# Optimization experiments

Measured on AMD Instinct MI355X. Metric: run time of the kernel, lower is better.

The kernel has to match this reference:

```python
import jax, jax.numpy as jnp
from jax import lax
import numpy as np

N = 227328   # B(32) * T(64) * 111 ROIs, block-diagonal collated graph
E = 1000000  # thresholded sparse edges
H = 128      # hidden_dim
NB = 111     # brain ROIs per graph (hardcoded in source)
P = 40       # |perm| (pooled node subset)
MAXLEN = 10  # max_path_length
NSTART = 5   # top-5 start nodes


def setup_inputs() -> dict:
    key = jax.random.key(0)
    ks = jax.random.split(key, 12)
    s = 1.0 / np.sqrt(H)
    return dict(
        v=jax.random.normal(ks[0], (N, H), jnp.float32),
        edge_row=jax.random.randint(ks[1], (E,), 0, N, jnp.int32),
        edge_col=jax.random.randint(ks[2], (E,), 0, N, jnp.int32),
        W1=jax.random.normal(ks[3], (H, H), jnp.float32) * s,
        b1=jnp.zeros((H,), jnp.float32),
        g1=jnp.ones((H,), jnp.float32),
        be1=jnp.zeros((H,), jnp.float32),
        W2=jax.random.normal(ks[4], (H, H), jnp.float32) * s,
        b2=jnp.zeros((H,), jnp.float32),
        g2=jnp.ones((H,), jnp.float32),
        be2=jnp.zeros((H,), jnp.float32),
        epsilon=jnp.zeros((1, 1), jnp.float32),
        adj111=jax.random.randint(ks[5], (NB, NB), 0, 2, jnp.int32),
        node_scores=jax.random.normal(ks[6], (NB,), jnp.float32),
        node_feats=jax.random.normal(ks[7], (NB, H), jnp.float32),
        perm=jnp.arange(P, dtype=jnp.int32),
        x_small=jax.random.normal(ks[8], (P, H), jnp.float32),
    )


def _batchnorm(x, g, b, eps=1e-5):
    # BatchNorm1d in training mode: biased batch statistics over node dim
    m = x.mean(0)
    var = x.var(0)
    return g * (x - m) * lax.rsqrt(var + eps) + b


def _gin(v, row, col, epsilon, W1, b1, g1, be1, W2, b2, g2, be2):
    # torch.sparse.mm(a, v): agg[i] = sum_{j: a[i,j]=1} v[j]
    agg = jax.ops.segment_sum(v[col], row, num_segments=v.shape[0])
    h = agg + epsilon[0, 0] * v
    h = jax.nn.relu(_batchnorm(h @ W1 + b1, g1, be1))
    h = jax.nn.relu(_batchnorm(h @ W2 + b2, g2, be2))
    return h


def _biased_random_walk(adj, scores, x, feats, perm):
    soft = jax.nn.softmax(scores)
    order = jnp.argsort(-scores)              # nodes by descending score
    in_perm = jnp.isin(order, perm)
    pos = jnp.where(in_perm, jnp.arange(NB), NB)
    starts = order[jnp.argsort(pos)[:NSTART]]  # first 5 sorted nodes in perm
    start_ok = jnp.arange(NSTART) < jnp.minimum(jnp.sum(in_perm), NSTART)

    def walk_one(carry, se):
        all_visited, xc = carry
        start, ok = se
        skip = jnp.logical_or(~ok, all_visited[start])
        visited0 = all_visited.at[start].set(True)

        def step(c, _):
            cur, visited, alive = c
            nbr = (adj[cur] > 0) & (~visited)
            has = jnp.any(nbr) & alive
            nxt = jnp.argmax(jnp.where(nbr, soft, -jnp.inf))  # greedy by softmax score
            cur2 = jnp.where(has, nxt, cur)
            visited2 = jnp.where(has, visited.at[nxt].set(True), visited)
            return (cur2, visited2, has), (cur2, has)

        (_, visited_f, _), (pn, pv) = lax.scan(
            step, (start, visited0, True), None, length=MAXLEN - 1)
        path = jnp.concatenate([start[None], pn])           # [MAXLEN]
        valid = jnp.concatenate([jnp.array([True]), pv])
        w = jax.nn.softmax(jnp.where(valid, scores[path], -jnp.inf))
        fused = jnp.sum(w[:, None] * feats[path], axis=0)   # [H]
        idx = jnp.argmax(perm == start)
        do = (~skip) & jnp.any(perm == start)
        x_new = jnp.where(do, xc.at[idx].add(fused), xc)
        av_new = jnp.where(skip, all_visited, visited_f)
        return (av_new, x_new), None

    (_, x_out), _ = lax.scan(
        walk_one, (jnp.zeros((NB,), bool), x), (starts, start_ok))
    return x_out


def reference(v, edge_row, edge_col, W1, b1, g1, be1, W2, b2, g2, be2,
              epsilon, adj111, node_scores, node_feats, perm, x_small):
    gin_out = _gin(v, edge_row, edge_col, epsilon,
                   W1, b1, g1, be1, W2, b2, g2, be2)
    x_fused = _biased_random_walk(adj111, node_scores, x_small,
                                  node_feats, perm)
    return gin_out, x_fused
```

## Files before the change

### kernel.cpp

```cpp
#include <hip/hip_runtime.h>
#include <hip/hip_bf16.h>
#include <math.h>

#define N_NODES 227328
#define H_DIM 128
#define NB_ 111
#define P_ 40
#define MAXLEN_ 10
#define NSTART_ 5
#define NH (N_NODES * H_DIM)
#define SCAN_BLK 1024

typedef __attribute__((ext_vector_type(8))) short short8;
typedef __attribute__((ext_vector_type(4))) float f32x4;


__global__ __launch_bounds__(256) void k_zero(float* wsf, int* cnt, int n) {
    int gstride = gridDim.x * blockDim.x;
    for (int i = blockIdx.x * blockDim.x + threadIdx.x; i < n; i += gstride) cnt[i] = 0;
    if (blockIdx.x == 0)
        for (int i = threadIdx.x; i < 1280; i += 256) wsf[i] = 0.f;
}


__global__ __launch_bounds__(256) void k_hist(const int* __restrict__ erow, int* cnt, int E) {
    int stride = gridDim.x * blockDim.x;
    for (int e = blockIdx.x * blockDim.x + threadIdx.x; e < E; e += stride)
        atomicAdd(&cnt[erow[e]], 1);
}

__global__ __launch_bounds__(256) void k_scan1(const int* __restrict__ cnt, int* __restrict__ ptr,
                                               int* __restrict__ bsum, int n) {
    __shared__ int s_warp[4];
    int t = threadIdx.x;
    int base = blockIdx.x * SCAN_BLK + t * 4;
    int x0 = (base + 0 < n) ? cnt[base + 0] : 0;
    int x1 = (base + 1 < n) ? cnt[base + 1] : 0;
    int x2 = (base + 2 < n) ? cnt[base + 2] : 0;
    int x3 = (base + 3 < n) ? cnt[base + 3] : 0;
    int tsum = x0 + x1 + x2 + x3;
    int lane = t & 63, w = t >> 6;
    int v = tsum;
#pragma unroll
    for (int m = 1; m < 64; m <<= 1) {
        int o = __shfl_up(v, m, 64);
        if (lane >= m) v += o;
    }
    if (lane == 63) s_warp[w] = v;
    __syncthreads();
    int wadd = 0;
    for (int j = 0; j < w; j++) wadd += s_warp[j];
    int excl = v - tsum + wadd;
    if (base + 0 < n) ptr[base + 0] = excl;
    if (base + 1 < n) ptr[base + 1] = excl + x0;
    if (base + 2 < n) ptr[base + 2] = excl + x0 + x1;
    if (base + 3 < n) ptr[base + 3] = excl + x0 + x1 + x2;
    if (t == 0) bsum[blockIdx.x] = s_warp[0] + s_warp[1] + s_warp[2] + s_warp[3];
}

__global__ __launch_bounds__(256) void k_scan2(int* bsum, int nb) {
    __shared__ int s[256];
    int t = threadIdx.x;
    s[t] = (t < nb) ? bsum[t] : 0;
    __syncthreads();
    if (t == 0) {
        int acc = 0;
        for (int i = 0; i < nb; i++) { int x = s[i]; s[i] = acc; acc += x; }
    }
    __syncthreads();
    if (t < nb) bsum[t] = s[t];
}

__global__ __launch_bounds__(256) void k_scan3(int* __restrict__ ptr, const int* __restrict__ bsum,
                                               int* __restrict__ cur, int n, int E) {
    int stride = gridDim.x * blockDim.x;
    for (int i = blockIdx.x * blockDim.x + threadIdx.x; i < n; i += stride) {
        int p = ptr[i] + bsum[i / SCAN_BLK];
        ptr[i] = p;
        cur[i] = p;
    }
    if (blockIdx.x == 0 && threadIdx.x == 0) ptr[n] = E;
}

__global__ __launch_bounds__(256) void k_fill(const int* __restrict__ erow,
                                              const int* __restrict__ ecol,
                                              int* cur, int* __restrict__ col, int E) {
    int stride = gridDim.x * blockDim.x;
    for (int e = blockIdx.x * blockDim.x + threadIdx.x; e < E; e += stride) {
        int p = atomicAdd(&cur[erow[e]], 1);
        col[p] = ecol[e];
    }
}

__global__ __launch_bounds__(256) void k_agg(const float* __restrict__ v,
                                             const int* __restrict__ ptr,
                                             const int* __restrict__ col,
                                             const float* __restrict__ epsp,
                                             float* __restrict__ out, int n) {
    int r = (blockIdx.x * 256 + threadIdx.x) >> 6;
    int lane = threadIdx.x & 63;
    if (r >= n) return;
    float eps = epsp[0];
    float2 a = *((const float2*)(v + (size_t)r * H_DIM) + lane);
    float acx = eps * a.x, acy = eps * a.y;
    int s = ptr[r], e = ptr[r + 1];
    int i = s;
    for (; i + 4 <= e; i += 4) {
        int c0 = col[i], c1 = col[i + 1], c2 = col[i + 2], c3 = col[i + 3];
        float2 b0 = *((const float2*)(v + (size_t)c0 * H_DIM) + lane);
        float2 b1 = *((const float2*)(v + (size_t)c1 * H_DIM) + lane);
        float2 b2 = *((const float2*)(v + (size_t)c2 * H_DIM) + lane);
        float2 b3 = *((const float2*)(v + (size_t)c3 * H_DIM) + lane);
        acx += (b0.x + b1.x) + (b2.x + b3.x);
        acy += (b0.y + b1.y) + (b2.y + b3.y);
    }
    for (; i < e; i++) {
        int c = col[i];
        float2 b = *((const float2*)(v + (size_t)c * H_DIM) + lane);
        acx += b.x;
        acy += b.y;
    }
    *((float2*)(out + (size_t)r * H_DIM) + lane) = make_float2(acx, acy);
}


__global__ __launch_bounds__(256) void k_init(const float4* __restrict__ v4,
                                              const float* __restrict__ epsp,
                                              float4* __restrict__ out4, int n4) {
    float eps = epsp[0];
    int stride = gridDim.x * blockDim.x;
    for (int i = blockIdx.x * blockDim.x + threadIdx.x; i < n4; i += stride) {
        float4 a = v4[i];
        out4[i] = make_float4(eps * a.x, eps * a.y, eps * a.z, eps * a.w);
    }
}

__global__ __launch_bounds__(256) void k_scatter(const float* __restrict__ v,
                                                 const int* __restrict__ erow,
                                                 const int* __restrict__ ecol,
                                                 float* agg, int E) {
    int tid = blockIdx.x * blockDim.x + threadIdx.x;
    int lane = tid & 63;
    int wave = tid >> 6;
    int nwaves = (gridDim.x * blockDim.x) >> 6;
    for (int e = wave; e < E; e += nwaves) {
        int r = erow[e], c = ecol[e];
        const float2 val = *((const float2*)(v + (size_t)c * H_DIM) + lane);
        float* dst = agg + (size_t)r * H_DIM + lane * 2;
        unsafeAtomicAdd(dst, val.x);
        unsafeAtomicAdd(dst + 1, val.y);
    }
}


__device__ inline void split8(const float* xs, short8& hi, short8& lo) {
#pragma unroll
    for (int e = 0; e < 8; e++) {
        unsigned u = __float_as_uint(xs[e]);
        hi[e] = (short)(unsigned short)(u >> 16);
        float hf = __uint_as_float(u & 0xFFFF0000u);
        lo[e] = (short)(unsigned short)(__float_as_uint(xs[e] - hf) >> 16);
    }
}

template <int BN>
__global__ __launch_bounds__(256, 2) void k_gemm_mfma(
        const float* __restrict__ A, float* __restrict__ C,
        const float* __restrict__ W, const float* __restrict__ bias,
        const float* __restrict__ scl_in, const float* __restrict__ of_in,
        float* __restrict__ sums, float* __restrict__ sumsq) {
    __shared__ unsigned short Whi[128 * 136];
    __shared__ unsigned short Wlo[128 * 136];
    __shared__ float scof[256];
    __shared__ float stats[2][4][128];

    const int t = threadIdx.x;
    const int w = t >> 6;
    const int l = t & 63;
    const int n = l & 15;
    const int g = l >> 4;
    const size_t row0 = (size_t)blockIdx.x * 128 + w * 32;

#pragma unroll 8
    for (int it = 0; it < 64; ++it) {
        int k = it * 2 + (t >> 7);
        int nn = t & 127;
        float wv = W[k * 128 + nn];
        unsigned u = __float_as_uint(wv);
        Whi[nn * 136 + k] = (unsigned short)(u >> 16);
        float hf = __uint_as_float(u & 0xFFFF0000u);
        Wlo[nn * 136 + k] = (unsigned short)(__float_as_uint(wv - hf) >> 16);
    }
    if (BN && t < 128) { scof[t] = scl_in[t]; scof[128 + t] = of_in[t]; }
    __syncthreads();

    float breg[8];
#pragma unroll
    for (int cb = 0; cb < 8; cb++) breg[cb] = bias[cb * 16 + n];

    f32x4 acc[2][8];
#pragma unroll
    for (int rf = 0; rf < 2; rf++)
#pragma unroll
        for (int cb = 0; cb < 8; cb++) acc[rf][cb] = (f32x4){0.f, 0.f, 0.f, 0.f};

    const float* Arow0 = A + (row0 + n) * H_DIM;
    const float* Arow1 = A + (row0 + 16 + n) * H_DIM;

#pragma unroll
    for (int kb = 0; kb < 4; kb++) {
        const int k0 = kb * 32 + g * 8;
        float4 x00 = *(const float4*)(Arow0 + k0);
        float4 x01 = *(const float4*)(Arow0 + k0 + 4);
        float4 x10 = *(const float4*)(Arow1 + k0);
        float4 x11 = *(const float4*)(Arow1 + k0 + 4);
        float xs0[8] = {x00.x, x00.y, x00.z, x00.w, x01.x, x01.y, x01.z, x01.w};
        float xs1[8] = {x10.x, x10.y, x10.z, x10.w, x11.x, x11.y, x11.z, x11.w};
        if (BN) {
            float sc[8], of[8];
            float4 sa = *(const float4*)(scof + k0);
            float4 sb = *(const float4*)(scof + k0 + 4);
            float4 oa = *(const float4*)(scof + 128 + k0);
            float4 ob = *(const float4*)(scof + 128 + k0 + 4);
            sc[0] = sa.x; sc[1] = sa.y; sc[2] = sa.z; sc[3] = sa.w;
            sc[4] = sb.x; sc[5] = sb.y; sc[6] = sb.z; sc[7] = sb.w;
            of[0] = oa.x; of[1] = oa.y; of[2] = oa.z; of[3] = oa.w;
            of[4] = ob.x; of[5] = ob.y; of[6] = ob.z; of[7] = ob.w;
#pragma unroll
            for (int e = 0; e < 8; e++) {
                xs0[e] = fmaxf(fmaf(xs0[e], sc[e], of[e]), 0.f);
                xs1[e] = fmaxf(fmaf(xs1[e], sc[e], of[e]), 0.f);
            }
        }
        short8 ah0, al0, ah1, al1;
        split8(xs0, ah0, al0);
        split8(xs1, ah1, al1);

        short8 wh[8], wl[8];
        const int wb = n * 136 + kb * 32 + g * 8;
#pragma unroll
        for (int cb = 0; cb < 8; cb++) {
            wh[cb] = *(const short8*)(Whi + cb * 2176 + wb);
            wl[cb] = *(const short8*)(Wlo + cb * 2176 + wb);
        }
#pragma unroll
        for (int cb = 0; cb < 8; cb++) {
            acc[0][cb] = __builtin_amdgcn_mfma_f32_16x16x32_bf16(ah0, wh[cb], acc[0][cb], 0, 0, 0);
            acc[1][cb] = __builtin_amdgcn_mfma_f32_16x16x32_bf16(ah1, wh[cb], acc[1][cb], 0, 0, 0);
            acc[0][cb] = __builtin_amdgcn_mfma_f32_16x16x32_bf16(al0, wh[cb], acc[0][cb], 0, 0, 0);
            acc[1][cb] = __builtin_amdgcn_mfma_f32_16x16x32_bf16(al1, wh[cb], acc[1][cb], 0, 0, 0);
            acc[0][cb] = __builtin_amdgcn_mfma_f32_16x16x32_bf16(ah0, wl[cb], acc[0][cb], 0, 0, 0);
            acc[1][cb] = __builtin_amdgcn_mfma_f32_16x16x32_bf16(ah1, wl[cb], acc[1][cb], 0, 0, 0);
        }
    }

    float s[8], s2[8];
#pragma unroll
    for (int cb = 0; cb < 8; cb++) { s[cb] = 0.f; s2[cb] = 0.f; }
#pragma unroll
    for (int cb = 0; cb < 8; cb++) {
        const int c = cb * 16 + n;
#pragma unroll
        for (int rf = 0; rf < 2; rf++) {
            f32x4 o = acc[rf][cb];
            const size_t rbase = (row0 + rf * 16 + g * 4) * H_DIM + c;
#pragma unroll
            for (int r = 0; r < 4; r++) {
                float val = o[r] + breg[cb];
                C[rbase + (size_t)r * H_DIM] = val;
                s[cb] += val;
                s2[cb] += val * val;
            }
        }
    }
#pragma unroll
    for (int cb = 0; cb < 8; cb++) {
        s[cb] += __shfl_xor(s[cb], 16, 64);
        s[cb] += __shfl_xor(s[cb], 32, 64);
        s2[cb] += __shfl_xor(s2[cb], 16, 64);
        s2[cb] += __shfl_xor(s2[cb], 32, 64);
    }
    if (g == 0) {
#pragma unroll
        for (int cb = 0; cb < 8; cb++) {
            stats[0][w][cb * 16 + n] = s[cb];
            stats[1][w][cb * 16 + n] = s2[cb];
        }
    }
    __syncthreads();
    if (t < 128) {
        float S  = stats[0][0][t] + stats[0][1][t] + stats[0][2][t] + stats[0][3][t];
        float S2 = stats[1][0][t] + stats[1][1][t] + stats[1][2][t] + stats[1][3][t];
        unsafeAtomicAdd(sums + t, S);
        unsafeAtomicAdd(sumsq + t, S2);
    }
}

__global__ void k_finalize(const float* __restrict__ sums, const float* __restrict__ sumsq,
                           float* __restrict__ mean, float* __restrict__ scl,
                           float* __restrict__ of,
                           const float* __restrict__ g, const float* __restrict__ beta,
                           float invN) {
    int t = threadIdx.x;
    if (t < H_DIM) {
        float m = sums[t] * invN;
        float var = sumsq[t] * invN - m * m;
        float sc = g[t] * rsqrtf(var + 1e-5f);
        mean[t] = m;
        scl[t] = sc;
        of[t] = beta[t] - m * sc;
    }
}


__device__ inline float block_max4(float v, int t, float* s_r) {
#pragma unroll
    for (int m = 1; m < 64; m <<= 1) v = fmaxf(v, __shfl_xor(v, m, 64));
    if ((t & 63) == 0) s_r[t >> 6] = v;
    __syncthreads();
    float r = fmaxf(fmaxf(s_r[0], s_r[1]), fmaxf(s_r[2], s_r[3]));
    __syncthreads();
    return r;
}

__device__ inline float block_sum4(float v, int t, float* s_r) {
#pragma unroll
    for (int m = 1; m < 64; m <<= 1) v += __shfl_xor(v, m, 64);
    if ((t & 63) == 0) s_r[t >> 6] = v;
    __syncthreads();
    float r = (s_r[0] + s_r[1]) + (s_r[2] + s_r[3]);
    __syncthreads();
    return r;
}

__device__ inline void block_argmax4(float v, int idx, int t, float* s_rv, int* s_ri,
                                     float* outv, int* outi) {
#pragma unroll
    for (int m = 1; m < 64; m <<= 1) {
        float ov = __shfl_xor(v, m, 64);
        int oi = __shfl_xor(idx, m, 64);
        if (ov > v || (ov == v && oi < idx)) { v = ov; idx = oi; }
    }
    if ((t & 63) == 0) { s_rv[t >> 6] = v; s_ri[t >> 6] = idx; }
    __syncthreads();
    float bv = s_rv[0];
    int bi = s_ri[0];
#pragma unroll
    for (int j = 1; j < 4; j++) {
        float ov = s_rv[j];
        int oi = s_ri[j];
        if (ov > bv || (ov == bv && oi < bi)) { bv = ov; bi = oi; }
    }
    *outv = bv;
    *outi = bi;
    __syncthreads();
}

__global__ __launch_bounds__(256) void k_bnwalk(
        float4* y4, const float* __restrict__ scl, const float* __restrict__ of, int n4,
        const int* __restrict__ adj, const float* __restrict__ scores,
        const float* __restrict__ feats, const int* __restrict__ perm,
        const float* __restrict__ xs, float* __restrict__ outw) {
    __shared__ int s_adj[NB_ * NB_];
    __shared__ float s_scores[NB_], s_soft[NB_];
    __shared__ int s_perm[P_];
    __shared__ unsigned char s_inperm[NB_], s_sel[NB_], s_allvis[NB_], s_vis[NB_];
    __shared__ int s_starts[NSTART_];
    __shared__ int s_path[MAXLEN_];
    __shared__ unsigned char s_valid[MAXLEN_];
    __shared__ float s_w[MAXLEN_];
    __shared__ int s_cur, s_alive, s_do, s_idx, s_skip;
    __shared__ float s_rv[4];
    __shared__ int s_ri[4];

    const int t = threadIdx.x;

    if (blockIdx.x != 0) {
        int stride = (gridDim.x - 1) * 256;
        for (int i = (blockIdx.x - 1) * 256 + t; i < n4; i += stride) {
            int c = (i & 31) * 4;
            float4 a = y4[i];
            a.x = fmaxf(fmaf(a.x, scl[c + 0], of[c + 0]), 0.f);
            a.y = fmaxf(fmaf(a.y, scl[c + 1], of[c + 1]), 0.f);
            a.z = fmaxf(fmaf(a.z, scl[c + 2], of[c + 2]), 0.f);
            a.w = fmaxf(fmaf(a.w, scl[c + 3], of[c + 3]), 0.f);
            y4[i] = a;
        }
        return;
    }

    for (int i = t; i < P_ * H_DIM; i += 256) outw[i] = xs[i];
    for (int i = t; i < NB_ * NB_; i += 256) s_adj[i] = adj[i];
    if (t < P_) s_perm[t] = perm[t];
    if (t < NB_) { s_scores[t] = scores[t]; s_allvis[t] = 0; s_sel[t] = 0; }
    __syncthreads();
    if (t < NB_) {
        unsigned char inp = 0;
        for (int j = 0; j < P_; j++) inp |= (s_perm[j] == t) ? 1 : 0;
        s_inperm[t] = inp;
    }
    __syncthreads();

    float myv = (t < NB_) ? s_scores[t] : -INFINITY;
    float mx = block_max4(myv, t, s_rv);
    float e = (t < NB_) ? expf(s_scores[t] - mx) : 0.f;
    float ssum = block_sum4(e, t, s_rv);
    if (t < NB_) s_soft[t] = e / ssum;

    float ninf = block_sum4((t < NB_ && s_inperm[t]) ? 1.f : 0.f, t, s_rv);
    int nin = (int)(ninf + 0.5f);
    int nok = nin < NSTART_ ? nin : NSTART_;
    __syncthreads();

    for (int r = 0; r < NSTART_; r++) {
        bool useIn = (r < nin);
        bool elig = (t < NB_) && !s_sel[t] && (((s_inperm[t] != 0)) == useIn);
        float v = elig ? s_scores[t] : -INFINITY;
        float mv; int mi;
        block_argmax4(v, elig ? t : 0x7fffffff, t, s_rv, s_ri, &mv, &mi);
        if (t == 0) s_starts[r] = mi;
        if (t == mi && t < NB_) s_sel[t] = 1;
        __syncthreads();
    }

    for (int s = 0; s < NSTART_; s++) {
        if (t == 0) {
            int start = s_starts[s];
            int ok = (s < nok) ? 1 : 0;
            int skip = (!ok) || s_allvis[start];
            s_skip = skip;
            s_cur = start;
            s_alive = 1;
            s_path[0] = start;
            s_valid[0] = 1;
            int idx = 0, found = 0;
            for (int j = 0; j < P_; j++)
                if (!found && s_perm[j] == start) { idx = j; found = 1; }
            s_idx = idx;
            s_do = (!skip) && found;
        }
        __syncthreads();
        if (t < NB_) s_vis[t] = s_allvis[t];
        __syncthreads();
        if (t == 0) s_vis[s_cur] = 1;
        __syncthreads();

        for (int st = 1; st < MAXLEN_; st++) {
            int cur = s_cur;
            int alive = s_alive;
            bool elig = (t < NB_) && alive && (s_adj[cur * NB_ + t] > 0) && (!s_vis[t]);
            float v = elig ? s_soft[t] : -INFINITY;
            float mv; int mi;
            block_argmax4(v, elig ? t : 0x7fffffff, t, s_rv, s_ri, &mv, &mi);
            if (t == 0) {
                int has = (mv > -INFINITY) ? 1 : 0;
                if (has) { s_cur = mi; s_vis[mi] = 1; }
                s_path[st] = has ? mi : cur;
                s_valid[st] = (unsigned char)has;
                s_alive = has;
            }
            __syncthreads();
        }

        if (t == 0) {
            float mxw = -INFINITY;
            for (int st = 0; st < MAXLEN_; st++)
                if (s_valid[st]) mxw = fmaxf(mxw, s_scores[s_path[st]]);
            float sw = 0.f;
            for (int st = 0; st < MAXLEN_; st++) {
                float ev = s_valid[st] ? expf(s_scores[s_path[st]] - mxw) : 0.f;
                s_w[st] = ev; sw += ev;
            }
            float inv = 1.f / sw;
            for (int st = 0; st < MAXLEN_; st++) s_w[st] *= inv;
        }
        __syncthreads();
        if (s_do && t < H_DIM) {
            float acc = 0.f;
            for (int st = 0; st < MAXLEN_; st++)
                acc += s_w[st] * feats[s_path[st] * H_DIM + t];
            outw[s_idx * H_DIM + t] += acc;
        }
        __syncthreads();
        if (!s_skip && t < NB_) s_allvis[t] = s_vis[t];
        __syncthreads();
    }
}


extern "C" void kernel_launch(void* const* d_in, const int* in_sizes, int n_in,
                              void* d_out, int out_size, void* d_ws, size_t ws_size,
                              hipStream_t stream) {
    const float* v    = (const float*)d_in[0];
    const int*   erow = (const int*)d_in[1];
    const int*   ecol = (const int*)d_in[2];
    const float* W1   = (const float*)d_in[3];
    const float* b1   = (const float*)d_in[4];
    const float* g1   = (const float*)d_in[5];
    const float* be1  = (const float*)d_in[6];
    const float* W2   = (const float*)d_in[7];
    const float* b2   = (const float*)d_in[8];
    const float* g2   = (const float*)d_in[9];
    const float* be2  = (const float*)d_in[10];
    const float* epsp = (const float*)d_in[11];
    const int*   adj  = (const int*)d_in[12];
    const float* scr  = (const float*)d_in[13];
    const float* fts  = (const float*)d_in[14];
    const int*   perm = (const int*)d_in[15];
    const float* xs   = (const float*)d_in[16];

    float* out = (float*)d_out;
    float* wsf = (float*)d_ws;
    float* sums1 = wsf,        *sumsq1 = wsf + 128,  *mean1 = wsf + 256,  *scl1 = wsf + 384,  *of1 = wsf + 512;
    float* sums2 = wsf + 640,  *sumsq2 = wsf + 768,  *mean2 = wsf + 896,  *scl2 = wsf + 1024, *of2 = wsf + 1152;

    const int E  = in_sizes[1];
    const int N  = N_NODES;
    const int n4 = NH / 4;

    int* ws_i = (int*)(wsf + 1280);
    int* cnt  = ws_i;
    int* ptr  = ws_i + (N + 1);
    int* cur  = ws_i + 2 * (N + 1);
    int* col  = ws_i + 3 * (N + 1);
    size_t need = 1280 * 4 + (size_t)(3 * (N + 1) + E) * 4;

    if (ws_size >= need) {
        const int nb = (N + SCAN_BLK - 1) / SCAN_BLK;
        k_zero<<<512, 256, 0, stream>>>(wsf, cnt, N + 1);
        k_hist<<<1024, 256, 0, stream>>>(erow, cnt, E);
        k_scan1<<<nb, 256, 0, stream>>>(cnt, ptr, cur , N);
        k_scan2<<<1, 256, 0, stream>>>(cur, nb);
        k_scan3<<<512, 256, 0, stream>>>(ptr, cur, cnt , N, E);
        k_fill<<<1024, 256, 0, stream>>>(erow, ecol, cnt, col, E);
        k_agg<<<N / 4, 256, 0, stream>>>(v, ptr, col, epsp, out, N);
    } else {
        k_zero<<<512, 256, 0, stream>>>(wsf, cnt, 0);
        k_init<<<2048, 256, 0, stream>>>((const float4*)v, epsp, (float4*)out, n4);
        k_scatter<<<4096, 256, 0, stream>>>(v, erow, ecol, out, E);
    }

    k_gemm_mfma<0><<<N / 128, 256, 0, stream>>>(out, out, W1, b1, nullptr, nullptr,
                                                sums1, sumsq1);
    k_finalize<<<1, 128, 0, stream>>>(sums1, sumsq1, mean1, scl1, of1, g1, be1, 1.f / N);
    k_gemm_mfma<1><<<N / 128, 256, 0, stream>>>(out, out, W2, b2, scl1, of1,
                                                sums2, sumsq2);
    k_finalize<<<1, 128, 0, stream>>>(sums2, sumsq2, mean2, scl2, of2, g2, be2, 1.f / N);
    k_bnwalk<<<2049, 256, 0, stream>>>((float4*)out, scl2, of2, n4,
                                       adj, scr, fts, perm, xs, out + NH);
}
```

Baseline: 655.5 us.

## Gather neighbor features from a bf16 copy and prefetch GEMM A tiles

Adds a kernel that converts v to a bf16 copy in workspace, and switches the CSR aggregation to gather neighbor rows from that copy with an 8-wide unroll, halving gather bytes per edge. The GEMM kernel now loads W with vectorized float4 reads and packed 32-bit LDS stores, and prefetches the next A k-slice into registers before the current MFMA block. The bf16 gather rounds neighbor features, which adds error to the aggregation relative to the fp32 reference. The extra conversion pass over v also costs bandwidth.

```diff
diff --git a/kernel.cpp b/kernel.cpp
--- a/kernel.cpp
+++ b/kernel.cpp
@@ -12,6 +12,7 @@
 #define SCAN_BLK 1024
 
 typedef __attribute__((ext_vector_type(8))) short short8;
+typedef __attribute__((ext_vector_type(8))) unsigned short ushort8;
 typedef __attribute__((ext_vector_type(4))) float f32x4;
 
 
@@ -20,6 +21,24 @@
     for (int i = blockIdx.x * blockDim.x + threadIdx.x; i < n; i += gstride) cnt[i] = 0;
     if (blockIdx.x == 0)
         for (int i = threadIdx.x; i < 1280; i += 256) wsf[i] = 0.f;
+}
+
+
+__device__ inline unsigned short f2bf(float x) {
+    unsigned u = __float_as_uint(x);
+    return (unsigned short)((u + 0x7FFFu + ((u >> 16) & 1u)) >> 16);
+}
+
+__global__ __launch_bounds__(256) void k_conv(const float4* __restrict__ v4,
+                                              ushort8* __restrict__ vb8, int n8) {
+    int stride = gridDim.x * blockDim.x;
+    for (int i = blockIdx.x * blockDim.x + threadIdx.x; i < n8; i += stride) {
+        float4 a = v4[i * 2], b = v4[i * 2 + 1];
+        ushort8 o;
+        o[0] = f2bf(a.x); o[1] = f2bf(a.y); o[2] = f2bf(a.z); o[3] = f2bf(a.w);
+        o[4] = f2bf(b.x); o[5] = f2bf(b.y); o[6] = f2bf(b.z); o[7] = f2bf(b.w);
+        vb8[i] = o;
+    }
 }
 
 
@@ -90,6 +109,54 @@
         int p = atomicAdd(&cur[erow[e]], 1);
         col[p] = ecol[e];
     }
+}
+
+
+__device__ inline float blo(unsigned u) { return __uint_as_float(u << 16); }
+__device__ inline float bhi(unsigned u) { return __uint_as_float(u & 0xFFFF0000u); }
+
+__global__ __launch_bounds__(256) void k_agg_bf16(const float* __restrict__ v,
+                                                  const unsigned* __restrict__ vbu,
+                                                  const int* __restrict__ ptr,
+                                                  const int* __restrict__ col,
+                                                  const float* __restrict__ epsp,
+                                                  float* __restrict__ out, int n) {
+    int r = (blockIdx.x * 256 + threadIdx.x) >> 6;
+    int lane = threadIdx.x & 63;
+    if (r >= n) return;
+    float eps = epsp[0];
+    float2 a = *((const float2*)(v + (size_t)r * H_DIM) + lane);
+    float acx = eps * a.x, acy = eps * a.y;
+    int s = ptr[r], e = ptr[r + 1];
+    int i = s;
+    for (; i + 8 <= e; i += 8) {
+        unsigned u0 = vbu[(size_t)col[i + 0] * 64 + lane];
+        unsigned u1 = vbu[(size_t)col[i + 1] * 64 + lane];
+        unsigned u2 = vbu[(size_t)col[i + 2] * 64 + lane];
+        unsigned u3 = vbu[(size_t)col[i + 3] * 64 + lane];
+        unsigned u4 = vbu[(size_t)col[i + 4] * 64 + lane];
+        unsigned u5 = vbu[(size_t)col[i + 5] * 64 + lane];
+        unsigned u6 = vbu[(size_t)col[i + 6] * 64 + lane];
+        unsigned u7 = vbu[(size_t)col[i + 7] * 64 + lane];
+        acx += ((blo(u0) + blo(u1)) + (blo(u2) + blo(u3))) +
+               ((blo(u4) + blo(u5)) + (blo(u6) + blo(u7)));
+        acy += ((bhi(u0) + bhi(u1)) + (bhi(u2) + bhi(u3))) +
+               ((bhi(u4) + bhi(u5)) + (bhi(u6) + bhi(u7)));
+    }
+    for (; i + 4 <= e; i += 4) {
+        unsigned u0 = vbu[(size_t)col[i + 0] * 64 + lane];
+        unsigned u1 = vbu[(size_t)col[i + 1] * 64 + lane];
+        unsigned u2 = vbu[(size_t)col[i + 2] * 64 + lane];
+        unsigned u3 = vbu[(size_t)col[i + 3] * 64 + lane];
+        acx += (blo(u0) + blo(u1)) + (blo(u2) + blo(u3));
+        acy += (bhi(u0) + bhi(u1)) + (bhi(u2) + bhi(u3));
+    }
+    for (; i < e; i++) {
+        unsigned u = vbu[(size_t)col[i] * 64 + lane];
+        acx += blo(u);
+        acy += bhi(u);
+    }
+    *((float2*)(out + (size_t)r * H_DIM) + lane) = make_float2(acx, acy);
 }
 
 __global__ __launch_bounds__(256) void k_agg(const float* __restrict__ v,
@@ -153,16 +220,6 @@
 }
 
 
-__device__ inline void split8(const float* xs, short8& hi, short8& lo) {
-#pragma unroll
-    for (int e = 0; e < 8; e++) {
-        unsigned u = __float_as_uint(xs[e]);
-        hi[e] = (short)(unsigned short)(u >> 16);
-        float hf = __uint_as_float(u & 0xFFFF0000u);
-        lo[e] = (short)(unsigned short)(__float_as_uint(xs[e] - hf) >> 16);
-    }
-}
-
 template <int BN>
 __global__ __launch_bounds__(256, 2) void k_gemm_mfma(
         const float* __restrict__ A, float* __restrict__ C,
@@ -181,39 +238,60 @@
     const int g = l >> 4;
     const size_t row0 = (size_t)blockIdx.x * 128 + w * 32;
 
-#pragma unroll 8
-    for (int it = 0; it < 64; ++it) {
-        int k = it * 2 + (t >> 7);
-        int nn = t & 127;
-        float wv = W[k * 128 + nn];
-        unsigned u = __float_as_uint(wv);
-        Whi[nn * 136 + k] = (unsigned short)(u >> 16);
-        float hf = __uint_as_float(u & 0xFFFF0000u);
-        Wlo[nn * 136 + k] = (unsigned short)(__float_as_uint(wv - hf) >> 16);
-    }
-    if (BN && t < 128) { scof[t] = scl_in[t]; scof[128 + t] = of_in[t]; }
-    __syncthreads();
-
-    float breg[8];
-#pragma unroll
-    for (int cb = 0; cb < 8; cb++) breg[cb] = bias[cb * 16 + n];
-
-    f32x4 acc[2][8];
-#pragma unroll
-    for (int rf = 0; rf < 2; rf++)
-#pragma unroll
-        for (int cb = 0; cb < 8; cb++) acc[rf][cb] = (f32x4){0.f, 0.f, 0.f, 0.f};
-
     const float* Arow0 = A + (row0 + n) * H_DIM;
     const float* Arow1 = A + (row0 + 16 + n) * H_DIM;
 
+    float4 x00 = *(const float4*)(Arow0 + g * 8);
+    float4 x01 = *(const float4*)(Arow0 + g * 8 + 4);
+    float4 x10 = *(const float4*)(Arow1 + g * 8);
+    float4 x11 = *(const float4*)(Arow1 + g * 8 + 4);
+
+#pragma unroll
+    for (int it = 0; it < 8; ++it) {
+        int p = it * 256 + t;
+        int k = (p >> 5) * 2;
+        int c = (p & 31) * 4;
+        float4 wa = *(const float4*)(W + k * 128 + c);
+        float4 wb = *(const float4*)(W + (k + 1) * 128 + c);
+        float fa[4] = {wa.x, wa.y, wa.z, wa.w};
+        float fb[4] = {wb.x, wb.y, wb.z, wb.w};
+#pragma unroll
+        for (int j = 0; j < 4; ++j) {
+            unsigned ua = __float_as_uint(fa[j]);
+            unsigned ub = __float_as_uint(fb[j]);
+            unsigned ha = ua >> 16, hb = ub >> 16;
+            float ra = fa[j] - __uint_as_float(ua & 0xFFFF0000u);
+            float rb = fb[j] - __uint_as_float(ub & 0xFFFF0000u);
+            unsigned la = __float_as_uint(ra) >> 16;
+            unsigned lb = __float_as_uint(rb) >> 16;
+            *(unsigned*)(&Whi[(c + j) * 136 + k]) = ha | (hb << 16);
+            *(unsigned*)(&Wlo[(c + j) * 136 + k]) = la | (lb << 16);
+        }
+    }
+    if (BN && t < 128) { scof[t] = scl_in[t]; scof[128 + t] = of_in[t]; }
+    __syncthreads();
+
+    float breg[8];
+#pragma unroll
+    for (int cb = 0; cb < 8; cb++) breg[cb] = bias[cb * 16 + n];
+
+    f32x4 acc[2][8];
+#pragma unroll
+    for (int rf = 0; rf < 2; rf++)
+#pragma unroll
+        for (int cb = 0; cb < 8; cb++) acc[rf][cb] = (f32x4){0.f, 0.f, 0.f, 0.f};
+
 #pragma unroll
     for (int kb = 0; kb < 4; kb++) {
+        float4 y00, y01, y10, y11;
+        if (kb < 3) {
+            const int kn = (kb + 1) * 32 + g * 8;
+            y00 = *(const float4*)(Arow0 + kn);
+            y01 = *(const float4*)(Arow0 + kn + 4);
+            y10 = *(const float4*)(Arow1 + kn);
+            y11 = *(const float4*)(Arow1 + kn + 4);
+        }
         const int k0 = kb * 32 + g * 8;
-        float4 x00 = *(const float4*)(Arow0 + k0);
-        float4 x01 = *(const float4*)(Arow0 + k0 + 4);
-        float4 x10 = *(const float4*)(Arow1 + k0);
-        float4 x11 = *(const float4*)(Arow1 + k0 + 4);
         float xs0[8] = {x00.x, x00.y, x00.z, x00.w, x01.x, x01.y, x01.z, x01.w};
         float xs1[8] = {x10.x, x10.y, x10.z, x10.w, x11.x, x11.y, x11.z, x11.w};
         if (BN) {
@@ -233,8 +311,15 @@
             }
         }
         short8 ah0, al0, ah1, al1;
-        split8(xs0, ah0, al0);
-        split8(xs1, ah1, al1);
+#pragma unroll
+        for (int e = 0; e < 8; e++) {
+            unsigned u0 = __float_as_uint(xs0[e]);
+            ah0[e] = (short)(unsigned short)(u0 >> 16);
+            al0[e] = (short)(unsigned short)(__float_as_uint(xs0[e] - __uint_as_float(u0 & 0xFFFF0000u)) >> 16);
+            unsigned u1 = __float_as_uint(xs1[e]);
+            ah1[e] = (short)(unsigned short)(u1 >> 16);
+            al1[e] = (short)(unsigned short)(__float_as_uint(xs1[e] - __uint_as_float(u1 & 0xFFFF0000u)) >> 16);
+        }
 
         short8 wh[8], wl[8];
         const int wb = n * 136 + kb * 32 + g * 8;
@@ -252,6 +337,7 @@
             acc[0][cb] = __builtin_amdgcn_mfma_f32_16x16x32_bf16(ah0, wl[cb], acc[0][cb], 0, 0, 0);
             acc[1][cb] = __builtin_amdgcn_mfma_f32_16x16x32_bf16(ah1, wl[cb], acc[1][cb], 0, 0, 0);
         }
+        x00 = y00; x01 = y01; x10 = y10; x11 = y11;
     }
 
     float s[8], s2[8];
@@ -523,17 +609,26 @@
     int* ptr  = ws_i + (N + 1);
     int* cur  = ws_i + 2 * (N + 1);
     int* col  = ws_i + 3 * (N + 1);
-    size_t need = 1280 * 4 + (size_t)(3 * (N + 1) + E) * 4;
-
-    if (ws_size >= need) {
+    size_t need_csr = 1280 * 4 + (size_t)(3 * (N + 1) + E) * 4;
+    size_t off_vb   = (need_csr + 15) & ~(size_t)15;
+    size_t need_vb  = off_vb + (size_t)NH * 2;
+    unsigned* vbu = (unsigned*)((char*)d_ws + off_vb);
+
+    if (ws_size >= need_csr) {
         const int nb = (N + SCAN_BLK - 1) / SCAN_BLK;
         k_zero<<<512, 256, 0, stream>>>(wsf, cnt, N + 1);
+        bool useBf = (ws_size >= need_vb);
+        if (useBf)
+            k_conv<<<2048, 256, 0, stream>>>((const float4*)v, (ushort8*)vbu, NH / 8);
         k_hist<<<1024, 256, 0, stream>>>(erow, cnt, E);
         k_scan1<<<nb, 256, 0, stream>>>(cnt, ptr, cur , N);
         k_scan2<<<1, 256, 0, stream>>>(cur, nb);
         k_scan3<<<512, 256, 0, stream>>>(ptr, cur, cnt , N, E);
         k_fill<<<1024, 256, 0, stream>>>(erow, ecol, cnt, col, E);
-        k_agg<<<N / 4, 256, 0, stream>>>(v, ptr, col, epsp, out, N);
+        if (useBf)
+            k_agg_bf16<<<N / 4, 256, 0, stream>>>(v, vbu, ptr, col, epsp, out, N);
+        else
+            k_agg<<<N / 4, 256, 0, stream>>>(v, ptr, col, epsp, out, N);
     } else {
         k_zero<<<512, 256, 0, stream>>>(wsf, cnt, 0);
         k_init<<<2048, 256, 0, stream>>>((const float4*)v, epsp, (float4*)out, n4);
```

After: 712.9 us. 8.8% more time.
